# Performance work log

Measured on AMD Instinct MI355X. Metric: run time of the kernel, lower is better.

The kernel has to match this reference:

```python
import jax, jax.numpy as jnp
import numpy as np

MAX_LEN = 96
Q_IDX = 0
U_IDX = 1
PROB_ADJ = 0.5


def setup_inputs() -> dict:
    key = jax.random.key(0)
    ks = jax.random.split(key, 12)
    B, H, V, I = 2048, 1024, 96, 1
    s = 1.0 / np.sqrt(H)
    u = lambda k, shape: jax.random.uniform(k, shape, jnp.float32, -s, s)
    return {
        "x": jax.random.normal(ks[0], (B, 1, MAX_LEN), jnp.float32),
        "l0_Wih": u(ks[1], (H, I)),
        "l0_Whh": u(ks[2], (H, H)),
        "l0_bih": u(ks[3], (H,)),
        "l0_bhh": u(ks[4], (H,)),
        "l1_Wih": u(ks[5], (H, H)),
        "l1_Whh": u(ks[6], (H, H)),
        "l1_bih": u(ks[7], (H,)),
        "l1_bhh": u(ks[8], (H,)),
        "fc_W": u(ks[9], (V, H)),
        "fc_b": u(ks[10], (V,)),
        "text_length": B,
    }


def reference(x, l0_Wih, l0_Whh, l0_bih, l0_bhh,
              l1_Wih, l1_Whh, l1_bih, l1_bhh, fc_W, fc_b, text_length):
    B = x.shape[0]
    H = l0_Whh.shape[0]
    # x: [B, 1, L] -> time-major sequence [L, B, 1]
    xs = jnp.transpose(x[:, 0, :], (1, 0))[:, :, None]
    h0 = jnp.zeros((B, H), x.dtype)
    h1 = jnp.zeros((B, H), x.dtype)

    def rnn_step(carry, xt):
        h0, h1 = carry
        h0 = jnp.tanh(xt @ l0_Wih.T + l0_bih + h0 @ l0_Whh.T + l0_bhh)
        h1 = jnp.tanh(h0 @ l1_Wih.T + l1_bih + h1 @ l1_Whh.T + l1_bhh)
        return (h0, h1), h1

    (h0, h1), hs = jax.lax.scan(rnn_step, (h0, h1), xs)  # hs: [L, B, H]
    logits = hs @ fc_W.T + fc_b  # [L, B, V]

    # In-place sequential probability patch: the k-th adjustment sees the
    # (k-1)-th row AFTER its adjustment, so scan carries the adjusted row.
    def adj_step(prev_row, inp):
        cur_row, is_last = inp
        prev_arg = jnp.argmax(prev_row, axis=-1)  # [B]
        cur_arg = jnp.argmax(cur_row, axis=-1)    # [B]
        cond_u = (prev_arg == Q_IDX) & (cur_arg != U_IDX)
        row = cur_row.at[:, U_IDX].add(jnp.where(cond_u, PROB_ADJ, 0.0))
        cond_q = is_last & (cur_arg == Q_IDX)
        row = row.at[:, Q_IDX].add(jnp.where(cond_q, -PROB_ADJ, 0.0))
        return row, row

    is_last = jnp.arange(1, MAX_LEN) == (MAX_LEN - 1)
    _, adjusted = jax.lax.scan(adj_step, logits[0], (logits[1:], is_last))
    outputs = jnp.concatenate([logits[:1], adjusted], axis=0)  # [L, B, V]
    outputs = jnp.transpose(outputs, (1, 0, 2))  # [B, L, V]
    hidden = jnp.stack([h0, h1], axis=0)  # [n_layers, B, H]
    return outputs, hidden
```

## Files before the change

### kernel.cpp

```cpp
#include <hip/hip_runtime.h>

#define Bn 2048
#define Hn 1024
#define Ln 96
#define Vn 96

typedef short bf16x8 __attribute__((ext_vector_type(8)));
typedef float f32x4 __attribute__((ext_vector_type(4)));

#define VM_WAIT(n) asm volatile("s_waitcnt vmcnt(" #n ")" ::: "memory")
#define BARRIER    asm volatile("s_barrier" ::: "memory")

__device__ __forceinline__ void async16(const void* g, void* l)
{
    __builtin_amdgcn_global_load_lds(
        (const __attribute__((address_space(1))) void*)g,
        (__attribute__((address_space(3))) void*)l, 16, 0, 0);
}

__device__ __forceinline__ unsigned short f2bf(float f)
{
    unsigned u = __float_as_uint(f);
    u += 0x7fff + ((u >> 16) & 1);
    return (unsigned short)(u >> 16);
}

__device__ __forceinline__ float bf2f(unsigned short s)
{
    return __uint_as_float(((unsigned)s) << 16);
}

__device__ __forceinline__ float fast_tanh(float x)
{
    float e = __expf(2.0f * x);
    return 1.0f - __fdividef(2.0f, e + 1.0f);
}

__global__ __launch_bounds__(512, 2) void fused_step(
    int s,
    const unsigned short* __restrict__ H0rd, unsigned short* __restrict__ H0wr,
    const unsigned short* __restrict__ H1rd, unsigned short* __restrict__ H1wr,
    const unsigned short* __restrict__ W0b,
    const unsigned short* __restrict__ W1ib, const unsigned short* __restrict__ W1hb,
    const unsigned short* __restrict__ fcWb,
    const float* __restrict__ w0ih,
    const float* __restrict__ b0i, const float* __restrict__ b0h,
    const float* __restrict__ b1i, const float* __restrict__ b1h,
    const float* __restrict__ fcb, const float* __restrict__ x,
    float* __restrict__ out)
{
    __shared__ __align__(16) unsigned short smem[32768];
    const int tid = threadIdx.x;
    const int lane = tid & 63;
    const int wave = tid >> 6;
    const int srow = lane >> 2;
    const int scol = ((lane & 3) ^ ((lane >> 3) & 3)) * 8;
    const int lr = lane & 15;
    const int lq = lane >> 4;
    const int roff = lr * 32 + ((lq ^ ((lr >> 1) & 3)) * 8);
    const int bid = blockIdx.x;

    if (bid < 128) {
        if (s < 1 || s > 96) return;
        const int bBase = (bid >> 3) * 128;
        const int iBase = (bid & 7) * 128;

        f32x4 acc[4][2];
#pragma unroll
        for (int i = 0; i < 4; ++i) {
            acc[i][0] = (f32x4){0.f, 0.f, 0.f, 0.f};
            acc[i][1] = (f32x4){0.f, 0.f, 0.f, 0.f};
        }
        const int mC = (wave >> 2) * 4;
        const int nC = (wave & 3) * 2;

        auto stage = [&](int ks, int buf) {
            const unsigned short* Ag = (ks < 16) ? H0rd : H1rd;
            const unsigned short* Bg = (ks < 16) ? W1ib : W1hb;
            const int koff = (ks & 15) * 64;
            if (wave < 4) {
#pragma unroll
                for (int j = 0; j < 4; ++j) {
                    const int id = wave * 4 + j;
                    const int c = id & 7, k2 = id >> 3;
                    async16(Ag + (size_t)(bBase + c * 16 + srow) * Hn + koff + k2 * 32 + scol,
                            smem + buf * 8192 + k2 * 4096 + c * 512);
                }
            } else {
#pragma unroll
                for (int j = 0; j < 4; ++j) {
                    const int id = (wave - 4) * 4 + j;
                    const int c = id & 7, k2 = id >> 3;
                    async16(Bg + (size_t)(iBase + c * 16 + srow) * Hn + koff + k2 * 32 + scol,
                            smem + 16384 + buf * 8192 + k2 * 4096 + c * 512);
                }
            }
        };

        stage(0, 0); VM_WAIT(0); BARRIER;
        for (int kc = 0; kc < 32; ++kc) {
            if (kc + 1 < 32) stage(kc + 1, (kc + 1) & 1);
            const int buf = kc & 1;
#pragma unroll
            for (int k2 = 0; k2 < 2; ++k2) {
                bf16x8 a[4], b[2];
#pragma unroll
                for (int mt = 0; mt < 4; ++mt)
                    a[mt] = *(const bf16x8*)(smem + buf * 8192 + k2 * 4096 + (mC + mt) * 512 + roff);
#pragma unroll
                for (int nt = 0; nt < 2; ++nt)
                    b[nt] = *(const bf16x8*)(smem + 16384 + buf * 8192 + k2 * 4096 + (nC + nt) * 512 + roff);
                __builtin_amdgcn_s_setprio(1);
#pragma unroll
                for (int mt = 0; mt < 4; ++mt)
#pragma unroll
                    for (int nt = 0; nt < 2; ++nt)
                        acc[mt][nt] = __builtin_amdgcn_mfma_f32_16x16x32_bf16(
                            a[mt], b[nt], acc[mt][nt], 0, 0, 0);
                __builtin_amdgcn_s_setprio(0);
            }
            VM_WAIT(0); BARRIER;
        }
        {
            const int mB = (wave >> 2) * 64;
            const int nB = (wave & 3) * 32;
#pragma unroll
            for (int nt = 0; nt < 2; ++nt) {
                const int n = iBase + nB + nt * 16 + lr;
                const float bs = b1i[n] + b1h[n];
#pragma unroll
                for (int mt = 0; mt < 4; ++mt)
#pragma unroll
                    for (int r = 0; r < 4; ++r) {
                        const int row = mB + mt * 16 + lq * 4 + r;
                        float v = acc[mt][nt][r] + bs;
                        H1wr[(size_t)(bBase + row) * Hn + n] = f2bf(fast_tanh(v));
                    }
            }
        }
    } else {
        const int idx = bid - 128;
        if (s <= 95) {
            const int bBase = (idx >> 3) * 128;
            const int iBase = (idx & 7) * 128;

            f32x4 acc[4][2];
#pragma unroll
            for (int i = 0; i < 4; ++i) {
                acc[i][0] = (f32x4){0.f, 0.f, 0.f, 0.f};
                acc[i][1] = (f32x4){0.f, 0.f, 0.f, 0.f};
            }
            const int mC = (wave >> 2) * 4;
            const int nC = (wave & 3) * 2;

            auto stage = [&](int ks, int buf) {
                const int koff = ks * 64;
                if (wave < 4) {
#pragma unroll
                    for (int j = 0; j < 4; ++j) {
                        const int id = wave * 4 + j;
                        const int c = id & 7, k2 = id >> 3;
                        async16(H0rd + (size_t)(bBase + c * 16 + srow) * Hn + koff + k2 * 32 + scol,
                                smem + buf * 8192 + k2 * 4096 + c * 512);
                    }
                } else {
#pragma unroll
                    for (int j = 0; j < 4; ++j) {
                        const int id = (wave - 4) * 4 + j;
                        const int c = id & 7, k2 = id >> 3;
                        async16(W0b + (size_t)(iBase + c * 16 + srow) * Hn + koff + k2 * 32 + scol,
                                smem + 16384 + buf * 8192 + k2 * 4096 + c * 512);
                    }
                }
            };

            stage(0, 0); VM_WAIT(0); BARRIER;
            for (int kc = 0; kc < 16; ++kc) {
                if (kc + 1 < 16) stage(kc + 1, (kc + 1) & 1);
                const int buf = kc & 1;
#pragma unroll
                for (int k2 = 0; k2 < 2; ++k2) {
                    bf16x8 a[4], b[2];
#pragma unroll
                    for (int mt = 0; mt < 4; ++mt)
                        a[mt] = *(const bf16x8*)(smem + buf * 8192 + k2 * 4096 + (mC + mt) * 512 + roff);
#pragma unroll
                    for (int nt = 0; nt < 2; ++nt)
                        b[nt] = *(const bf16x8*)(smem + 16384 + buf * 8192 + k2 * 4096 + (nC + nt) * 512 + roff);
                    __builtin_amdgcn_s_setprio(1);
#pragma unroll
                    for (int mt = 0; mt < 4; ++mt)
#pragma unroll
                        for (int nt = 0; nt < 2; ++nt)
                            acc[mt][nt] = __builtin_amdgcn_mfma_f32_16x16x32_bf16(
                                a[mt], b[nt], acc[mt][nt], 0, 0, 0);
                    __builtin_amdgcn_s_setprio(0);
                }
                VM_WAIT(0); BARRIER;
            }
            {
                const int mB = (wave >> 2) * 64;
                const int nB = (wave & 3) * 32;
#pragma unroll
                for (int nt = 0; nt < 2; ++nt) {
                    const int n = iBase + nB + nt * 16 + lr;
                    const float wv = w0ih[n];
                    const float bs = b0i[n] + b0h[n];
#pragma unroll
                    for (int mt = 0; mt < 4; ++mt)
#pragma unroll
                        for (int r = 0; r < 4; ++r) {
                            const int row = mB + mt * 16 + lq * 4 + r;
                            const int bb = bBase + row;
                            const float xv = x[bb * Ln + s];
                            float v = acc[mt][nt][r] + xv * wv + bs;
                            H0wr[(size_t)bb * Hn + n] = f2bf(fast_tanh(v));
                        }
                }
            }
        }
        if (idx < 16 && s >= 2) {
            __syncthreads();
            const int t = s - 2;
            const int bBase2 = idx * 128;

            f32x4 acc2[2][3];
#pragma unroll
            for (int i = 0; i < 2; ++i)
#pragma unroll
                for (int j = 0; j < 3; ++j) acc2[i][j] = (f32x4){0.f, 0.f, 0.f, 0.f};
            const int mC2 = (wave >> 1) * 2;
            const int nC2 = (wave & 1) * 3;

            auto stageF = [&](int ks, int buf) {
                const int koff = ks * 64;
                if (wave < 4) {
#pragma unroll
                    for (int j = 0; j < 4; ++j) {
                        const int id = wave * 4 + j;
                        const int c = id & 7, k2 = id >> 3;
                        async16(H1rd + (size_t)(bBase2 + c * 16 + srow) * Hn + koff + k2 * 32 + scol,
                                smem + buf * 8192 + k2 * 4096 + c * 512);
                    }
                } else if (wave < 7) {
#pragma unroll
                    for (int j = 0; j < 4; ++j) {
                        const int id = (wave - 4) * 4 + j;
                        const int k2 = id / 6, c = id % 6;
                        async16(fcWb + (size_t)(c * 16 + srow) * Hn + koff + k2 * 32 + scol,
                                smem + 16384 + buf * 8192 + k2 * 4096 + c * 512);
                    }
                }
            };

            stageF(0, 0); VM_WAIT(0); BARRIER;
            for (int kc = 0; kc < 16; ++kc) {
                if (kc + 1 < 16) stageF(kc + 1, (kc + 1) & 1);
                const int buf = kc & 1;
#pragma unroll
                for (int k2 = 0; k2 < 2; ++k2) {
                    bf16x8 a[2], b[3];
#pragma unroll
                    for (int mt = 0; mt < 2; ++mt)
                        a[mt] = *(const bf16x8*)(smem + buf * 8192 + k2 * 4096 + (mC2 + mt) * 512 + roff);
#pragma unroll
                    for (int nt = 0; nt < 3; ++nt)
                        b[nt] = *(const bf16x8*)(smem + 16384 + buf * 8192 + k2 * 4096 + (nC2 + nt) * 512 + roff);
                    __builtin_amdgcn_s_setprio(1);
#pragma unroll
                    for (int mt = 0; mt < 2; ++mt)
#pragma unroll
                        for (int nt = 0; nt < 3; ++nt)
                            acc2[mt][nt] = __builtin_amdgcn_mfma_f32_16x16x32_bf16(
                                a[mt], b[nt], acc2[mt][nt], 0, 0, 0);
                    __builtin_amdgcn_s_setprio(0);
                }
                VM_WAIT(0); BARRIER;
            }
            {
                const int mB2 = (wave >> 1) * 32;
                const int nB2 = (wave & 1) * 48;
#pragma unroll
                for (int mt = 0; mt < 2; ++mt)
#pragma unroll
                    for (int r = 0; r < 4; ++r) {
                        const int row = mB2 + mt * 16 + lq * 4 + r;
                        const size_t o = (size_t)(bBase2 + row) * (Ln * Vn) + (size_t)t * Vn;
#pragma unroll
                        for (int nt = 0; nt < 3; ++nt) {
                            const int n = nB2 + nt * 16 + lr;
                            out[o + n] = acc2[mt][nt][r] + fcb[n];
                        }
                    }
            }
        }
    }
}

__global__ void f32_to_bf16(const float* __restrict__ in,
                            unsigned short* __restrict__ out, int n)
{
    int i = blockIdx.x * blockDim.x + threadIdx.x;
    int stride = gridDim.x * blockDim.x;
    for (; i < n; i += stride) out[i] = f2bf(in[i]);
}

__global__ void hidden_out(const unsigned short* __restrict__ h0,
                           const unsigned short* __restrict__ h1,
                           float* __restrict__ out)
{
    int i = blockIdx.x * 256 + threadIdx.x;
    out[i] = bf2f(h0[i]);
    out[(size_t)Bn * Hn + i] = bf2f(h1[i]);
}

__global__ __launch_bounds__(128) void adjust_kernel(float* __restrict__ out)
{
    __shared__ float s_mex[Ln], s_v0[Ln], s_v1[Ln];
    __shared__ int   s_iex[Ln];
    const int b = blockIdx.x;
    const int t = threadIdx.x;
    float* row = out + (size_t)b * (Ln * Vn);

    if (t < Ln) {
        const float4* r4 = (const float4*)(row + t * Vn);
        float4 q = r4[0];
        float m = q.x; int im = 0;
        if (q.z > m) { m = q.z; im = 2; }
        if (q.w > m) { m = q.w; im = 3; }
        const float v0 = q.x, v1 = q.y;
        for (int jj = 1; jj < 24; ++jj) {
            float4 p = r4[jj];
            const int base = jj * 4;
            if (p.x > m) { m = p.x; im = base; }
            if (p.y > m) { m = p.y; im = base + 1; }
            if (p.z > m) { m = p.z; im = base + 2; }
            if (p.w > m) { m = p.w; im = base + 3; }
        }
        s_mex[t] = m; s_iex[t] = im; s_v0[t] = v0; s_v1[t] = v1;
    }
    __syncthreads();

    if (t == 0) {
        float v1p = s_v1[0]; float mp = s_mex[0]; int ip = s_iex[0];
        int prev = (v1p > mp || (v1p == mp && ip != 0)) ? 1 : ip;
        for (int k = 1; k < Ln; ++k) {
            const float v1c = s_v1[k];
            const float mc = s_mex[k];
            const int ic = s_iex[k];
            const int cur = (v1c > mc || (v1c == mc && ic != 0)) ? 1 : ic;
            float v1a = v1c;
            if (prev == 0 && cur != 1) {
                v1a = v1c + 0.5f;
                row[k * Vn + 1] = v1a;
            }
            if (k == Ln - 1 && cur == 0)
                row[k * Vn + 0] = s_v0[k] - 0.5f;
            prev = (v1a > mc || (v1a == mc && ic != 0)) ? 1 : ic;
        }
    }
}

extern "C" void kernel_launch(void* const* d_in, const int* in_sizes, int n_in,
                              void* d_out, int out_size, void* d_ws, size_t ws_size,
                              hipStream_t stream)
{
    const float* x    = (const float*)d_in[0];
    const float* w0ih = (const float*)d_in[1];
    const float* W0   = (const float*)d_in[2];
    const float* b0i  = (const float*)d_in[3];
    const float* b0h  = (const float*)d_in[4];
    const float* W1i  = (const float*)d_in[5];
    const float* W1h  = (const float*)d_in[6];
    const float* b1i  = (const float*)d_in[7];
    const float* b1h  = (const float*)d_in[8];
    const float* fcW  = (const float*)d_in[9];
    const float* fcb  = (const float*)d_in[10];
    float* out = (float*)d_out;

    const size_t HH = (size_t)Hn * Hn;
    const size_t BH = (size_t)Bn * Hn;
    unsigned short* ws = (unsigned short*)d_ws;
    unsigned short* W0b  = ws;
    unsigned short* W1ib = ws + HH;
    unsigned short* W1hb = ws + 2 * HH;
    unsigned short* fcWb = ws + 3 * HH;
    unsigned short* H0[2] = { ws + 4 * HH,          ws + 4 * HH + BH };
    unsigned short* H1[2] = { ws + 4 * HH + 2 * BH, ws + 4 * HH + 3 * BH };

    hipMemsetAsync(H0[0], 0, BH * sizeof(unsigned short), stream);
    hipMemsetAsync(H1[0], 0, BH * sizeof(unsigned short), stream);

    f32_to_bf16<<<dim3(512), dim3(256), 0, stream>>>(W0,  W0b,  (int)HH);
    f32_to_bf16<<<dim3(512), dim3(256), 0, stream>>>(W1i, W1ib, (int)HH);
    f32_to_bf16<<<dim3(512), dim3(256), 0, stream>>>(W1h, W1hb, (int)HH);
    f32_to_bf16<<<dim3(64),  dim3(256), 0, stream>>>(fcW, fcWb, Vn * Hn);

    for (int s = 0; s <= 97; ++s) {
        fused_step<<<dim3(256), dim3(512), 0, stream>>>(
            s,
            H0[s & 1], H0[(s + 1) & 1],
            H1[(s + 1) & 1], H1[s & 1],
            W0b, W1ib, W1hb, fcWb,
            w0ih, b0i, b0h, b1i, b1h, fcb, x, out);
    }

    adjust_kernel<<<dim3(Bn), dim3(128), 0, stream>>>(out);

    hidden_out<<<dim3((int)(BH / 256)), dim3(256), 0, stream>>>(
        H0[0], H1[0], out + (size_t)Bn * Ln * Vn);
}
```

Before: 2.879 ms.

## Split-K across wave halves with 64x64 wave tiles and triple-buffered loads

The layer GEMM tiles now give each wave a 64x64 output tile, with the two halves of the block each taking one k-half of every 64-wide chunk. Partial sums are reduced through shared memory before the tanh epilogue. Global-to-LDS staging moves from double to triple buffering, with a partial vmcnt wait so loads run two chunks ahead. Weight conversion and hidden-state zeroing are folded into one prep kernel. This raises LDS to 96KB and drops launch bounds to one block per CU, trading occupancy for more MFMA work per LDS read and better load overlap.

```diff
diff --git a/kernel.cpp b/kernel.cpp
--- a/kernel.cpp
+++ b/kernel.cpp
@@ -36,7 +36,7 @@
     return 1.0f - __fdividef(2.0f, e + 1.0f);
 }
 
-__global__ __launch_bounds__(512, 2) void fused_step(
+__global__ __launch_bounds__(512, 1) void fused_step(
     int s,
     const unsigned short* __restrict__ H0rd, unsigned short* __restrict__ H0wr,
     const unsigned short* __restrict__ H1rd, unsigned short* __restrict__ H1wr,
@@ -49,7 +49,7 @@
     const float* __restrict__ fcb, const float* __restrict__ x,
     float* __restrict__ out)
 {
-    __shared__ __align__(16) unsigned short smem[32768];
+    __shared__ __align__(16) unsigned short smem[49152];
     const int tid = threadIdx.x;
     const int lane = tid & 63;
     const int wave = tid >> 6;
@@ -60,24 +60,37 @@
     const int roff = lr * 32 + ((lq ^ ((lr >> 1) & 3)) * 8);
     const int bid = blockIdx.x;
 
-    if (bid < 128) {
-        if (s < 1 || s > 96) return;
-        const int bBase = (bid >> 3) * 128;
-        const int iBase = (bid & 7) * 128;
-
-        f32x4 acc[4][2];
-#pragma unroll
-        for (int i = 0; i < 4; ++i) {
-            acc[i][0] = (f32x4){0.f, 0.f, 0.f, 0.f};
-            acc[i][1] = (f32x4){0.f, 0.f, 0.f, 0.f};
-        }
-        const int mC = (wave >> 2) * 4;
-        const int nC = (wave & 3) * 2;
+    const bool isL1 = (bid < 128);
+    const int idx = bid & 127;
+    const bool doMain = isL1 ? (s >= 1 && s <= 96) : (s <= 95);
+
+    const int half = wave >> 2;
+    const int qm = (wave >> 1) & 1;
+    const int qn = wave & 1;
+    const int qoff = ((qm << 1) | qn) * (64 * 66);
+
+    if (doMain) {
+        const int bBase = (idx >> 3) * 128;
+        const int iBase = (idx & 7) * 128;
+        const int NIT = isL1 ? 32 : 16;
+
+        f32x4 acc[4][4];
+#pragma unroll
+        for (int i = 0; i < 4; ++i)
+#pragma unroll
+            for (int j = 0; j < 4; ++j) acc[i][j] = (f32x4){0.f, 0.f, 0.f, 0.f};
 
         auto stage = [&](int ks, int buf) {
-            const unsigned short* Ag = (ks < 16) ? H0rd : H1rd;
-            const unsigned short* Bg = (ks < 16) ? W1ib : W1hb;
-            const int koff = (ks & 15) * 64;
+            const unsigned short* Ag;
+            const unsigned short* Bg;
+            int koff;
+            if (isL1) {
+                Ag = (ks < 16) ? H0rd : H1rd;
+                Bg = (ks < 16) ? W1ib : W1hb;
+                koff = (ks & 15) * 64;
+            } else {
+                Ag = H0rd; Bg = W0b; koff = ks * 64;
+            }
             if (wave < 4) {
 #pragma unroll
                 for (int j = 0; j < 4; ++j) {
@@ -92,217 +105,183 @@
                     const int id = (wave - 4) * 4 + j;
                     const int c = id & 7, k2 = id >> 3;
                     async16(Bg + (size_t)(iBase + c * 16 + srow) * Hn + koff + k2 * 32 + scol,
-                            smem + 16384 + buf * 8192 + k2 * 4096 + c * 512);
+                            smem + 24576 + buf * 8192 + k2 * 4096 + c * 512);
                 }
             }
         };
 
-        stage(0, 0); VM_WAIT(0); BARRIER;
-        for (int kc = 0; kc < 32; ++kc) {
-            if (kc + 1 < 32) stage(kc + 1, (kc + 1) & 1);
-            const int buf = kc & 1;
-#pragma unroll
-            for (int k2 = 0; k2 < 2; ++k2) {
-                bf16x8 a[4], b[2];
-#pragma unroll
-                for (int mt = 0; mt < 4; ++mt)
-                    a[mt] = *(const bf16x8*)(smem + buf * 8192 + k2 * 4096 + (mC + mt) * 512 + roff);
-#pragma unroll
-                for (int nt = 0; nt < 2; ++nt)
-                    b[nt] = *(const bf16x8*)(smem + 16384 + buf * 8192 + k2 * 4096 + (nC + nt) * 512 + roff);
-                __builtin_amdgcn_s_setprio(1);
-#pragma unroll
-                for (int mt = 0; mt < 4; ++mt)
-#pragma unroll
-                    for (int nt = 0; nt < 2; ++nt)
-                        acc[mt][nt] = __builtin_amdgcn_mfma_f32_16x16x32_bf16(
-                            a[mt], b[nt], acc[mt][nt], 0, 0, 0);
-                __builtin_amdgcn_s_setprio(0);
-            }
-            VM_WAIT(0); BARRIER;
-        }
-        {
-            const int mB = (wave >> 2) * 64;
-            const int nB = (wave & 3) * 32;
-#pragma unroll
-            for (int nt = 0; nt < 2; ++nt) {
-                const int n = iBase + nB + nt * 16 + lr;
-                const float bs = b1i[n] + b1h[n];
-#pragma unroll
-                for (int mt = 0; mt < 4; ++mt)
-#pragma unroll
-                    for (int r = 0; r < 4; ++r) {
-                        const int row = mB + mt * 16 + lq * 4 + r;
-                        float v = acc[mt][nt][r] + bs;
-                        H1wr[(size_t)(bBase + row) * Hn + n] = f2bf(fast_tanh(v));
-                    }
-            }
-        }
-    } else {
-        const int idx = bid - 128;
-        if (s <= 95) {
-            const int bBase = (idx >> 3) * 128;
-            const int iBase = (idx & 7) * 128;
-
-            f32x4 acc[4][2];
-#pragma unroll
-            for (int i = 0; i < 4; ++i) {
-                acc[i][0] = (f32x4){0.f, 0.f, 0.f, 0.f};
-                acc[i][1] = (f32x4){0.f, 0.f, 0.f, 0.f};
-            }
-            const int mC = (wave >> 2) * 4;
-            const int nC = (wave & 3) * 2;
-
-            auto stage = [&](int ks, int buf) {
-                const int koff = ks * 64;
-                if (wave < 4) {
-#pragma unroll
-                    for (int j = 0; j < 4; ++j) {
-                        const int id = wave * 4 + j;
-                        const int c = id & 7, k2 = id >> 3;
-                        async16(H0rd + (size_t)(bBase + c * 16 + srow) * Hn + koff + k2 * 32 + scol,
-                                smem + buf * 8192 + k2 * 4096 + c * 512);
-                    }
-                } else {
-#pragma unroll
-                    for (int j = 0; j < 4; ++j) {
-                        const int id = (wave - 4) * 4 + j;
-                        const int c = id & 7, k2 = id >> 3;
-                        async16(W0b + (size_t)(iBase + c * 16 + srow) * Hn + koff + k2 * 32 + scol,
-                                smem + 16384 + buf * 8192 + k2 * 4096 + c * 512);
-                    }
-                }
-            };
-
-            stage(0, 0); VM_WAIT(0); BARRIER;
-            for (int kc = 0; kc < 16; ++kc) {
-                if (kc + 1 < 16) stage(kc + 1, (kc + 1) & 1);
-                const int buf = kc & 1;
-#pragma unroll
-                for (int k2 = 0; k2 < 2; ++k2) {
-                    bf16x8 a[4], b[2];
+        stage(0, 0); stage(1, 1);
+        for (int kc = 0; kc < NIT; ++kc) {
+            if (kc + 1 < NIT) VM_WAIT(4);
+            else              VM_WAIT(0);
+            BARRIER;
+            const int cb = kc % 3;
+            if (kc + 2 < NIT) stage(kc + 2, (kc + 2) % 3);
+            bf16x8 a[4], b[4];
+#pragma unroll
+            for (int i = 0; i < 4; ++i)
+                a[i] = *(const bf16x8*)(smem + cb * 8192 + half * 4096 + (qm * 4 + i) * 512 + roff);
+#pragma unroll
+            for (int i = 0; i < 4; ++i)
+                b[i] = *(const bf16x8*)(smem + 24576 + cb * 8192 + half * 4096 + (qn * 4 + i) * 512 + roff);
+            __builtin_amdgcn_s_setprio(1);
+#pragma unroll
+            for (int mt = 0; mt < 4; ++mt)
+#pragma unroll
+                for (int nt = 0; nt < 4; ++nt)
+                    acc[mt][nt] = __builtin_amdgcn_mfma_f32_16x16x32_bf16(
+                        a[mt], b[nt], acc[mt][nt], 0, 0, 0);
+            __builtin_amdgcn_s_setprio(0);
+        }
+
+        __syncthreads();
+        float* red = (float*)smem;
+        if (wave < 4) {
+#pragma unroll
+            for (int mt = 0; mt < 4; ++mt)
+#pragma unroll
+                for (int nt = 0; nt < 4; ++nt)
+#pragma unroll
+                    for (int r = 0; r < 4; ++r)
+                        red[qoff + (mt * 16 + lq * 4 + r) * 66 + nt * 16 + lr] = acc[mt][nt][r];
+        }
+        __syncthreads();
+        if (wave >= 4) {
+            if (isL1) {
+#pragma unroll
+                for (int nt = 0; nt < 4; ++nt) {
+                    const int n = iBase + qn * 64 + nt * 16 + lr;
+                    const float bs = b1i[n] + b1h[n];
 #pragma unroll
                     for (int mt = 0; mt < 4; ++mt)
-                        a[mt] = *(const bf16x8*)(smem + buf * 8192 + k2 * 4096 + (mC + mt) * 512 + roff);
-#pragma unroll
-                    for (int nt = 0; nt < 2; ++nt)
-                        b[nt] = *(const bf16x8*)(smem + 16384 + buf * 8192 + k2 * 4096 + (nC + nt) * 512 + roff);
-                    __builtin_amdgcn_s_setprio(1);
-#pragma unroll
-                    for (int mt = 0; mt < 4; ++mt)
-#pragma unroll
-                        for (int nt = 0; nt < 2; ++nt)
-                            acc[mt][nt] = __builtin_amdgcn_mfma_f32_16x16x32_bf16(
-                                a[mt], b[nt], acc[mt][nt], 0, 0, 0);
-                    __builtin_amdgcn_s_setprio(0);
-                }
-                VM_WAIT(0); BARRIER;
-            }
-            {
-                const int mB = (wave >> 2) * 64;
-                const int nB = (wave & 3) * 32;
-#pragma unroll
-                for (int nt = 0; nt < 2; ++nt) {
-                    const int n = iBase + nB + nt * 16 + lr;
+#pragma unroll
+                        for (int r = 0; r < 4; ++r) {
+                            const int rl = mt * 16 + lq * 4 + r;
+                            float v = acc[mt][nt][r] + red[qoff + rl * 66 + nt * 16 + lr] + bs;
+                            H1wr[(size_t)(bBase + qm * 64 + rl) * Hn + n] = f2bf(fast_tanh(v));
+                        }
+                }
+            } else {
+#pragma unroll
+                for (int nt = 0; nt < 4; ++nt) {
+                    const int n = iBase + qn * 64 + nt * 16 + lr;
                     const float wv = w0ih[n];
                     const float bs = b0i[n] + b0h[n];
 #pragma unroll
                     for (int mt = 0; mt < 4; ++mt)
 #pragma unroll
                         for (int r = 0; r < 4; ++r) {
-                            const int row = mB + mt * 16 + lq * 4 + r;
-                            const int bb = bBase + row;
+                            const int rl = mt * 16 + lq * 4 + r;
+                            const int bb = bBase + qm * 64 + rl;
                             const float xv = x[bb * Ln + s];
-                            float v = acc[mt][nt][r] + xv * wv + bs;
+                            float v = acc[mt][nt][r] + red[qoff + rl * 66 + nt * 16 + lr] + xv * wv + bs;
                             H0wr[(size_t)bb * Hn + n] = f2bf(fast_tanh(v));
                         }
                 }
             }
         }
-        if (idx < 16 && s >= 2) {
-            __syncthreads();
-            const int t = s - 2;
-            const int bBase2 = idx * 128;
-
-            f32x4 acc2[2][3];
-#pragma unroll
-            for (int i = 0; i < 2; ++i)
-#pragma unroll
-                for (int j = 0; j < 3; ++j) acc2[i][j] = (f32x4){0.f, 0.f, 0.f, 0.f};
-            const int mC2 = (wave >> 1) * 2;
-            const int nC2 = (wave & 1) * 3;
-
-            auto stageF = [&](int ks, int buf) {
-                const int koff = ks * 64;
-                if (wave < 4) {
-#pragma unroll
-                    for (int j = 0; j < 4; ++j) {
-                        const int id = wave * 4 + j;
-                        const int c = id & 7, k2 = id >> 3;
-                        async16(H1rd + (size_t)(bBase2 + c * 16 + srow) * Hn + koff + k2 * 32 + scol,
-                                smem + buf * 8192 + k2 * 4096 + c * 512);
+    }
+
+    if (!isL1 && idx < 16 && s >= 2) {
+        if (doMain) __syncthreads();
+        const int t = s - 2;
+        const int bBase2 = idx * 128;
+
+        f32x4 acc2[2][3];
+#pragma unroll
+        for (int i = 0; i < 2; ++i)
+#pragma unroll
+            for (int j = 0; j < 3; ++j) acc2[i][j] = (f32x4){0.f, 0.f, 0.f, 0.f};
+        const int mC2 = (wave >> 1) * 2;
+        const int nC2 = (wave & 1) * 3;
+
+        auto stageF = [&](int ks, int buf) {
+            const int koff = ks * 64;
+            if (wave < 4) {
+#pragma unroll
+                for (int j = 0; j < 4; ++j) {
+                    const int id = wave * 4 + j;
+                    const int c = id & 7, k2 = id >> 3;
+                    async16(H1rd + (size_t)(bBase2 + c * 16 + srow) * Hn + koff + k2 * 32 + scol,
+                            smem + buf * 8192 + k2 * 4096 + c * 512);
+                }
+            } else if (wave < 7) {
+#pragma unroll
+                for (int j = 0; j < 4; ++j) {
+                    const int id = (wave - 4) * 4 + j;
+                    const int k2 = id / 6, c = id % 6;
+                    async16(fcWb + (size_t)(c * 16 + srow) * Hn + koff + k2 * 32 + scol,
+                            smem + 24576 + buf * 8192 + k2 * 4096 + c * 512);
+                }
+            }
+        };
+
+        stageF(0, 0); stageF(1, 1);
+        for (int kc = 0; kc < 16; ++kc) {
+            if (kc + 1 < 16) VM_WAIT(4);
+            else             VM_WAIT(0);
+            BARRIER;
+            const int cb = kc % 3;
+            if (kc + 2 < 16) stageF(kc + 2, (kc + 2) % 3);
+#pragma unroll
+            for (int k2 = 0; k2 < 2; ++k2) {
+                bf16x8 a[2], b[3];
+#pragma unroll
+                for (int mt = 0; mt < 2; ++mt)
+                    a[mt] = *(const bf16x8*)(smem + cb * 8192 + k2 * 4096 + (mC2 + mt) * 512 + roff);
+#pragma unroll
+                for (int nt = 0; nt < 3; ++nt)
+                    b[nt] = *(const bf16x8*)(smem + 24576 + cb * 8192 + k2 * 4096 + (nC2 + nt) * 512 + roff);
+                __builtin_amdgcn_s_setprio(1);
+#pragma unroll
+                for (int mt = 0; mt < 2; ++mt)
+#pragma unroll
+                    for (int nt = 0; nt < 3; ++nt)
+                        acc2[mt][nt] = __builtin_amdgcn_mfma_f32_16x16x32_bf16(
+                            a[mt], b[nt], acc2[mt][nt], 0, 0, 0);
+                __builtin_amdgcn_s_setprio(0);
+            }
+        }
+        {
+            const int mB2 = (wave >> 1) * 32;
+            const int nB2 = (wave & 1) * 48;
+#pragma unroll
+            for (int mt = 0; mt < 2; ++mt)
+#pragma unroll
+                for (int r = 0; r < 4; ++r) {
+                    const int row = mB2 + mt * 16 + lq * 4 + r;
+                    const size_t o = (size_t)(bBase2 + row) * (Ln * Vn) + (size_t)t * Vn;
+#pragma unroll
+                    for (int nt = 0; nt < 3; ++nt) {
+                        const int n = nB2 + nt * 16 + lr;
+                        out[o + n] = acc2[mt][nt][r] + fcb[n];
                     }
-                } else if (wave < 7) {
-#pragma unroll
-                    for (int j = 0; j < 4; ++j) {
-                        const int id = (wave - 4) * 4 + j;
-                        const int k2 = id / 6, c = id % 6;
-                        async16(fcWb + (size_t)(c * 16 + srow) * Hn + koff + k2 * 32 + scol,
-                                smem + 16384 + buf * 8192 + k2 * 4096 + c * 512);
-                    }
-                }
-            };
-
-            stageF(0, 0); VM_WAIT(0); BARRIER;
-            for (int kc = 0; kc < 16; ++kc) {
-                if (kc + 1 < 16) stageF(kc + 1, (kc + 1) & 1);
-                const int buf = kc & 1;
-#pragma unroll
-                for (int k2 = 0; k2 < 2; ++k2) {
-                    bf16x8 a[2], b[3];
-#pragma unroll
-                    for (int mt = 0; mt < 2; ++mt)
-                        a[mt] = *(const bf16x8*)(smem + buf * 8192 + k2 * 4096 + (mC2 + mt) * 512 + roff);
-#pragma unroll
-                    for (int nt = 0; nt < 3; ++nt)
-                        b[nt] = *(const bf16x8*)(smem + 16384 + buf * 8192 + k2 * 4096 + (nC2 + nt) * 512 + roff);
-                    __builtin_amdgcn_s_setprio(1);
-#pragma unroll
-                    for (int mt = 0; mt < 2; ++mt)
-#pragma unroll
-                        for (int nt = 0; nt < 3; ++nt)
-                            acc2[mt][nt] = __builtin_amdgcn_mfma_f32_16x16x32_bf16(
-                                a[mt], b[nt], acc2[mt][nt], 0, 0, 0);
-                    __builtin_amdgcn_s_setprio(0);
-                }
-                VM_WAIT(0); BARRIER;
-            }
-            {
-                const int mB2 = (wave >> 1) * 32;
-                const int nB2 = (wave & 1) * 48;
-#pragma unroll
-                for (int mt = 0; mt < 2; ++mt)
-#pragma unroll
-                    for (int r = 0; r < 4; ++r) {
-                        const int row = mB2 + mt * 16 + lq * 4 + r;
-                        const size_t o = (size_t)(bBase2 + row) * (Ln * Vn) + (size_t)t * Vn;
-#pragma unroll
-                        for (int nt = 0; nt < 3; ++nt) {
-                            const int n = nB2 + nt * 16 + lr;
-                            out[o + n] = acc2[mt][nt][r] + fcb[n];
-                        }
-                    }
-            }
-        }
-    }
-}
-
-__global__ void f32_to_bf16(const float* __restrict__ in,
-                            unsigned short* __restrict__ out, int n)
-{
+                }
+        }
+    }
+}
+
+__global__ void prep_kernel(const float* __restrict__ W0, const float* __restrict__ W1i,
+                            const float* __restrict__ W1h, const float* __restrict__ fcW,
+                            unsigned short* __restrict__ W0b, unsigned short* __restrict__ W1ib,
+                            unsigned short* __restrict__ W1hb, unsigned short* __restrict__ fcWb,
+                            unsigned short* __restrict__ H0z, unsigned short* __restrict__ H1z)
+{
+    const int HH = Hn * Hn;
+    const int VH = Vn * Hn;
+    const int BH = Bn * Hn;
+    const int nconv = 3 * HH + VH;
+    const int total = nconv + 2 * BH;
     int i = blockIdx.x * blockDim.x + threadIdx.x;
-    int stride = gridDim.x * blockDim.x;
-    for (; i < n; i += stride) out[i] = f2bf(in[i]);
+    const int stride = gridDim.x * blockDim.x;
+    for (; i < total; i += stride) {
+        if (i < HH)            W0b[i] = f2bf(W0[i]);
+        else if (i < 2 * HH)   W1ib[i - HH] = f2bf(W1i[i - HH]);
+        else if (i < 3 * HH)   W1hb[i - 2 * HH] = f2bf(W1h[i - 2 * HH]);
+        else if (i < nconv)    fcWb[i - 3 * HH] = f2bf(fcW[i - 3 * HH]);
+        else if (i < nconv + BH) H0z[i - nconv] = 0;
+        else                   H1z[i - nconv - BH] = 0;
+    }
 }
 
 __global__ void hidden_out(const unsigned short* __restrict__ h0,
@@ -388,13 +367,8 @@
     unsigned short* H0[2] = { ws + 4 * HH,          ws + 4 * HH + BH };
     unsigned short* H1[2] = { ws + 4 * HH + 2 * BH, ws + 4 * HH + 3 * BH };
 
-    hipMemsetAsync(H0[0], 0, BH * sizeof(unsigned short), stream);
-    hipMemsetAsync(H1[0], 0, BH * sizeof(unsigned short), stream);
-
-    f32_to_bf16<<<dim3(512), dim3(256), 0, stream>>>(W0,  W0b,  (int)HH);
-    f32_to_bf16<<<dim3(512), dim3(256), 0, stream>>>(W1i, W1ib, (int)HH);
-    f32_to_bf16<<<dim3(512), dim3(256), 0, stream>>>(W1h, W1hb, (int)HH);
-    f32_to_bf16<<<dim3(64),  dim3(256), 0, stream>>>(fcW, fcWb, Vn * Hn);
+    prep_kernel<<<dim3(1024), dim3(256), 0, stream>>>(
+        W0, W1i, W1h, fcW, W0b, W1ib, W1hb, fcWb, H0[0], H1[0]);
 
     for (int s = 0; s <= 97; ++s) {
         fused_step<<<dim3(256), dim3(512), 0, stream>>>(
```

Measured after the change: 3.502 ms. +21.6%, slower.

## Double K-chunk per stage to halve barriers; fuse weight conversion and zeroing

Applied to the files above, without the earlier changes.

Each GEMM stage in the fused step kernel now loads a 128-wide K chunk instead of 64. This doubles shared memory to 128 KB, halves the number of pipeline iterations and barrier/wait points, and drops the occupancy target from 2 blocks to 1 per CU. The weight-to-bf16 conversions and the hidden-state memsets are merged into a single prep kernel to cut launch overhead. The risk is lower occupancy, which leaves less latency hiding across blocks.

```diff
diff --git a/kernel.cpp b/kernel.cpp
--- a/kernel.cpp
+++ b/kernel.cpp
@@ -36,7 +36,7 @@
     return 1.0f - __fdividef(2.0f, e + 1.0f);
 }
 
-__global__ __launch_bounds__(512, 2) void fused_step(
+__global__ __launch_bounds__(512, 1) void fused_step(
     int s,
     const unsigned short* __restrict__ H0rd, unsigned short* __restrict__ H0wr,
     const unsigned short* __restrict__ H1rd, unsigned short* __restrict__ H1wr,
@@ -49,7 +49,7 @@
     const float* __restrict__ fcb, const float* __restrict__ x,
     float* __restrict__ out)
 {
-    __shared__ __align__(16) unsigned short smem[32768];
+    __shared__ __align__(16) unsigned short smem[65536];
     const int tid = threadIdx.x;
     const int lane = tid & 63;
     const int wave = tid >> 6;
@@ -75,41 +75,35 @@
         const int nC = (wave & 3) * 2;
 
         auto stage = [&](int ks, int buf) {
-            const unsigned short* Ag = (ks < 16) ? H0rd : H1rd;
-            const unsigned short* Bg = (ks < 16) ? W1ib : W1hb;
-            const int koff = (ks & 15) * 64;
+            const unsigned short* Ag = (ks < 8) ? H0rd : H1rd;
+            const unsigned short* Bg = (ks < 8) ? W1ib : W1hb;
+            const int koff = (ks & 7) * 128;
             if (wave < 4) {
 #pragma unroll
-                for (int j = 0; j < 4; ++j) {
-                    const int id = wave * 4 + j;
-                    const int c = id & 7, k2 = id >> 3;
-                    async16(Ag + (size_t)(bBase + c * 16 + srow) * Hn + koff + k2 * 32 + scol,
-                            smem + buf * 8192 + k2 * 4096 + c * 512);
-                }
+                for (int j = 0; j < 8; ++j)
+                    async16(Ag + (size_t)(bBase + j * 16 + srow) * Hn + koff + wave * 32 + scol,
+                            smem + buf * 16384 + wave * 4096 + j * 512);
             } else {
 #pragma unroll
-                for (int j = 0; j < 4; ++j) {
-                    const int id = (wave - 4) * 4 + j;
-                    const int c = id & 7, k2 = id >> 3;
-                    async16(Bg + (size_t)(iBase + c * 16 + srow) * Hn + koff + k2 * 32 + scol,
-                            smem + 16384 + buf * 8192 + k2 * 4096 + c * 512);
-                }
+                for (int j = 0; j < 8; ++j)
+                    async16(Bg + (size_t)(iBase + j * 16 + srow) * Hn + koff + (wave - 4) * 32 + scol,
+                            smem + 32768 + buf * 16384 + (wave - 4) * 4096 + j * 512);
             }
         };
 
         stage(0, 0); VM_WAIT(0); BARRIER;
-        for (int kc = 0; kc < 32; ++kc) {
-            if (kc + 1 < 32) stage(kc + 1, (kc + 1) & 1);
+        for (int kc = 0; kc < 16; ++kc) {
+            if (kc + 1 < 16) stage(kc + 1, (kc + 1) & 1);
             const int buf = kc & 1;
 #pragma unroll
-            for (int k2 = 0; k2 < 2; ++k2) {
+            for (int k2 = 0; k2 < 4; ++k2) {
                 bf16x8 a[4], b[2];
 #pragma unroll
                 for (int mt = 0; mt < 4; ++mt)
-                    a[mt] = *(const bf16x8*)(smem + buf * 8192 + k2 * 4096 + (mC + mt) * 512 + roff);
+                    a[mt] = *(const bf16x8*)(smem + buf * 16384 + k2 * 4096 + (mC + mt) * 512 + roff);
 #pragma unroll
                 for (int nt = 0; nt < 2; ++nt)
-                    b[nt] = *(const bf16x8*)(smem + 16384 + buf * 8192 + k2 * 4096 + (nC + nt) * 512 + roff);
+                    b[nt] = *(const bf16x8*)(smem + 32768 + buf * 16384 + k2 * 4096 + (nC + nt) * 512 + roff);
                 __builtin_amdgcn_s_setprio(1);
 #pragma unroll
                 for (int mt = 0; mt < 4; ++mt)
@@ -154,39 +148,33 @@
             const int nC = (wave & 3) * 2;
 
             auto stage = [&](int ks, int buf) {
-                const int koff = ks * 64;
+                const int koff = ks * 128;
                 if (wave < 4) {
 #pragma unroll
-                    for (int j = 0; j < 4; ++j) {
-                        const int id = wave * 4 + j;
-                        const int c = id & 7, k2 = id >> 3;
-                        async16(H0rd + (size_t)(bBase + c * 16 + srow) * Hn + koff + k2 * 32 + scol,
-                                smem + buf * 8192 + k2 * 4096 + c * 512);
-                    }
+                    for (int j = 0; j < 8; ++j)
+                        async16(H0rd + (size_t)(bBase + j * 16 + srow) * Hn + koff + wave * 32 + scol,
+                                smem + buf * 16384 + wave * 4096 + j * 512);
                 } else {
 #pragma unroll
-                    for (int j = 0; j < 4; ++j) {
-                        const int id = (wave - 4) * 4 + j;
-                        const int c = id & 7, k2 = id >> 3;
-                        async16(W0b + (size_t)(iBase + c * 16 + srow) * Hn + koff + k2 * 32 + scol,
-                                smem + 16384 + buf * 8192 + k2 * 4096 + c * 512);
-                    }
+                    for (int j = 0; j < 8; ++j)
+                        async16(W0b + (size_t)(iBase + j * 16 + srow) * Hn + koff + (wave - 4) * 32 + scol,
+                                smem + 32768 + buf * 16384 + (wave - 4) * 4096 + j * 512);
                 }
             };
 
             stage(0, 0); VM_WAIT(0); BARRIER;
-            for (int kc = 0; kc < 16; ++kc) {
-                if (kc + 1 < 16) stage(kc + 1, (kc + 1) & 1);
+            for (int kc = 0; kc < 8; ++kc) {
+                if (kc + 1 < 8) stage(kc + 1, (kc + 1) & 1);
                 const int buf = kc & 1;
 #pragma unroll
-                for (int k2 = 0; k2 < 2; ++k2) {
+                for (int k2 = 0; k2 < 4; ++k2) {
                     bf16x8 a[4], b[2];
 #pragma unroll
                     for (int mt = 0; mt < 4; ++mt)
-                        a[mt] = *(const bf16x8*)(smem + buf * 8192 + k2 * 4096 + (mC + mt) * 512 + roff);
+                        a[mt] = *(const bf16x8*)(smem + buf * 16384 + k2 * 4096 + (mC + mt) * 512 + roff);
 #pragma unroll
                     for (int nt = 0; nt < 2; ++nt)
-                        b[nt] = *(const bf16x8*)(smem + 16384 + buf * 8192 + k2 * 4096 + (nC + nt) * 512 + roff);
+                        b[nt] = *(const bf16x8*)(smem + 32768 + buf * 16384 + k2 * 4096 + (nC + nt) * 512 + roff);
                     __builtin_amdgcn_s_setprio(1);
 #pragma unroll
                     for (int mt = 0; mt < 4; ++mt)
@@ -233,39 +221,36 @@
             const int nC2 = (wave & 1) * 3;
 
             auto stageF = [&](int ks, int buf) {
-                const int koff = ks * 64;
+                const int koff = ks * 128;
                 if (wave < 4) {
 #pragma unroll
-                    for (int j = 0; j < 4; ++j) {
-                        const int id = wave * 4 + j;
-                        const int c = id & 7, k2 = id >> 3;
-                        async16(H1rd + (size_t)(bBase2 + c * 16 + srow) * Hn + koff + k2 * 32 + scol,
-                                smem + buf * 8192 + k2 * 4096 + c * 512);
-                    }
-                } else if (wave < 7) {
-#pragma unroll
-                    for (int j = 0; j < 4; ++j) {
-                        const int id = (wave - 4) * 4 + j;
+                    for (int j = 0; j < 8; ++j)
+                        async16(H1rd + (size_t)(bBase2 + j * 16 + srow) * Hn + koff + wave * 32 + scol,
+                                smem + buf * 16384 + wave * 4096 + j * 512);
+                } else {
+#pragma unroll
+                    for (int j = 0; j < 6; ++j) {
+                        const int id = (wave - 4) * 6 + j;
                         const int k2 = id / 6, c = id % 6;
                         async16(fcWb + (size_t)(c * 16 + srow) * Hn + koff + k2 * 32 + scol,
-                                smem + 16384 + buf * 8192 + k2 * 4096 + c * 512);
+                                smem + 32768 + buf * 12288 + k2 * 3072 + c * 512);
                     }
                 }
             };
 
             stageF(0, 0); VM_WAIT(0); BARRIER;
-            for (int kc = 0; kc < 16; ++kc) {
-                if (kc + 1 < 16) stageF(kc + 1, (kc + 1) & 1);
+            for (int kc = 0; kc < 8; ++kc) {
+                if (kc + 1 < 8) stageF(kc + 1, (kc + 1) & 1);
                 const int buf = kc & 1;
 #pragma unroll
-                for (int k2 = 0; k2 < 2; ++k2) {
+                for (int k2 = 0; k2 < 4; ++k2) {
                     bf16x8 a[2], b[3];
 #pragma unroll
                     for (int mt = 0; mt < 2; ++mt)
-                        a[mt] = *(const bf16x8*)(smem + buf * 8192 + k2 * 4096 + (mC2 + mt) * 512 + roff);
+                        a[mt] = *(const bf16x8*)(smem + buf * 16384 + k2 * 4096 + (mC2 + mt) * 512 + roff);
 #pragma unroll
                     for (int nt = 0; nt < 3; ++nt)
-                        b[nt] = *(const bf16x8*)(smem + 16384 + buf * 8192 + k2 * 4096 + (nC2 + nt) * 512 + roff);
+                        b[nt] = *(const bf16x8*)(smem + 32768 + buf * 12288 + k2 * 3072 + (nC2 + nt) * 512 + roff);
                     __builtin_amdgcn_s_setprio(1);
 #pragma unroll
                     for (int mt = 0; mt < 2; ++mt)
@@ -297,12 +282,27 @@
     }
 }
 
-__global__ void f32_to_bf16(const float* __restrict__ in,
-                            unsigned short* __restrict__ out, int n)
-{
+__global__ void prep_kernel(const float* __restrict__ W0, const float* __restrict__ W1i,
+                            const float* __restrict__ W1h, const float* __restrict__ fcW,
+                            unsigned short* __restrict__ W0b, unsigned short* __restrict__ W1ib,
+                            unsigned short* __restrict__ W1hb, unsigned short* __restrict__ fcWb,
+                            unsigned short* __restrict__ H0z, unsigned short* __restrict__ H1z)
+{
+    const int HH = Hn * Hn;
+    const int VH = Vn * Hn;
+    const int BH = Bn * Hn;
+    const int nconv = 3 * HH + VH;
+    const int total = nconv + 2 * BH;
     int i = blockIdx.x * blockDim.x + threadIdx.x;
-    int stride = gridDim.x * blockDim.x;
-    for (; i < n; i += stride) out[i] = f2bf(in[i]);
+    const int stride = gridDim.x * blockDim.x;
+    for (; i < total; i += stride) {
+        if (i < HH)            W0b[i] = f2bf(W0[i]);
+        else if (i < 2 * HH)   W1ib[i - HH] = f2bf(W1i[i - HH]);
+        else if (i < 3 * HH)   W1hb[i - 2 * HH] = f2bf(W1h[i - 2 * HH]);
+        else if (i < nconv)    fcWb[i - 3 * HH] = f2bf(fcW[i - 3 * HH]);
+        else if (i < nconv + BH) H0z[i - nconv] = 0;
+        else                   H1z[i - nconv - BH] = 0;
+    }
 }
 
 __global__ void hidden_out(const unsigned short* __restrict__ h0,
@@ -388,13 +388,8 @@
     unsigned short* H0[2] = { ws + 4 * HH,          ws + 4 * HH + BH };
     unsigned short* H1[2] = { ws + 4 * HH + 2 * BH, ws + 4 * HH + 3 * BH };
 
-    hipMemsetAsync(H0[0], 0, BH * sizeof(unsigned short), stream);
-    hipMemsetAsync(H1[0], 0, BH * sizeof(unsigned short), stream);
-
-    f32_to_bf16<<<dim3(512), dim3(256), 0, stream>>>(W0,  W0b,  (int)HH);
-    f32_to_bf16<<<dim3(512), dim3(256), 0, stream>>>(W1i, W1ib, (int)HH);
-    f32_to_bf16<<<dim3(512), dim3(256), 0, stream>>>(W1h, W1hb, (int)HH);
-    f32_to_bf16<<<dim3(64),  dim3(256), 0, stream>>>(fcW, fcWb, Vn * Hn);
+    prep_kernel<<<dim3(1024), dim3(256), 0, stream>>>(
+        W0, W1i, W1h, fcW, W0b, W1ib, W1hb, fcWb, H0[0], H1[0]);
 
     for (int s = 0; s <= 97; ++s) {
         fused_step<<<dim3(256), dim3(512), 0, stream>>>(
```

After: 2.433 ms. -15.5%, faster.
